# Kernel optimization log

Measured on AMD Instinct MI355X. Metric: run time of the kernel, lower is better.

The kernel has to match this reference:

```python
import jax, jax.numpy as jnp
import numpy as np

N_X, DIS, IN, OUT = 40000, 10000, 128, 64
N = N_X + DIS
E = 800000
BN_EPS = 1e-5


def setup_inputs() -> dict:
    key = jax.random.key(0)
    ks = jax.random.split(key, 20)

    def glorot(k, shape):
        fan_in, fan_out = shape[-2], shape[-1]
        a = np.sqrt(6.0 / (fan_in + fan_out)).astype(np.float32)
        return jax.random.uniform(k, shape, jnp.float32, -a, a)

    return {
        "x": jax.random.normal(ks[0], (N_X, IN), jnp.float32),
        "emb": jax.random.uniform(ks[1], (DIS, IN), jnp.float32),
        "conv1_w": glorot(ks[2], (3, IN, 2 * OUT)),
        "conv1_root": glorot(ks[3], (IN, 2 * OUT)),
        "conv1_bias": jnp.zeros((2 * OUT,), jnp.float32),
        "conv2_w": glorot(ks[4], (3, 2 * OUT, 4 * OUT)),
        "conv2_root": glorot(ks[5], (2 * OUT, 4 * OUT)),
        "conv2_bias": jnp.zeros((4 * OUT,), jnp.float32),
        "convinf_w": glorot(ks[6], (3, 4 * OUT, 4 * OUT)),
        "convinf_root": glorot(ks[7], (4 * OUT, 4 * OUT)),
        "convinf_bias": jnp.zeros((4 * OUT,), jnp.float32),
        "conv3_w": glorot(ks[8], (3, 4 * OUT, OUT)),
        "conv3_root": glorot(ks[9], (4 * OUT, OUT)),
        "conv3_bias": jnp.zeros((OUT,), jnp.float32),
        "norm1_g": jnp.ones((2 * OUT,), jnp.float32),
        "norm1_b": jnp.zeros((2 * OUT,), jnp.float32),
        "norm2_g": jnp.ones((4 * OUT,), jnp.float32),
        "norm2_b": jnp.zeros((4 * OUT,), jnp.float32),
        "edge_index": jax.random.randint(ks[10], (2, E), 0, N),
        "edge_types": jax.random.randint(ks[11], (E,), 0, 3),
    }


def reference(x, emb, conv1_w, conv1_root, conv1_bias, conv2_w, conv2_root,
              conv2_bias, convinf_w, convinf_root, convinf_bias, conv3_w,
              conv3_root, conv3_bias, norm1_g, norm1_b, norm2_g, norm2_b,
              edge_index, edge_types):
    dst, src = edge_index[0], edge_index[1]  # adj_t row = target, col = source
    n = x.shape[0] + emb.shape[0]

    # gcn_norm without self-loops: deg over rows, w_e = d^-1/2[dst] * d^-1/2[src]
    deg = jax.ops.segment_sum(jnp.ones(dst.shape[0], jnp.float32), dst, num_segments=n)
    dis = jnp.where(deg > 0, jax.lax.rsqrt(jnp.maximum(deg, 1.0)), 0.0)
    ew = dis[dst] * dis[src]  # [E]

    def wrgcn(h, W, root, bias):
        out = h @ root + bias
        h_src = h[src]  # [E, d] gather (dominant memory traffic)
        for r in range(3):
            w_r = jnp.where(edge_types == r, ew, 0.0)
            agg = jax.ops.segment_sum(w_r[:, None] * h_src, dst, num_segments=n)
            out = out + agg @ W[r]
        return out

    def bn(h, g, b):
        m = h.mean(axis=0)
        v = jnp.var(h, axis=0)  # biased, matches torch BN training normalization
        return (h - m) * jax.lax.rsqrt(v + BN_EPS) * g + b

    h0 = jnp.concatenate([x, emb], axis=0)  # [N, IN]
    x1 = bn(wrgcn(h0, conv1_w, conv1_root, conv1_bias), norm1_g, norm1_b)
    x2 = bn(wrgcn(jax.nn.relu(x1), conv2_w, conv2_root, conv2_bias), norm2_g, norm2_b)
    for _ in range(5):
        x2 = bn(wrgcn(jax.nn.relu(x2), convinf_w, convinf_root, convinf_bias), norm2_g, norm2_b)
    return wrgcn(jax.nn.relu(x2), conv3_w, conv3_root, conv3_bias)
```

## Files before the change

### kernel.cpp

```cpp
#include <hip/hip_runtime.h>

#define N_X  40000
#define NN   50000
#define NE   800000
#define MPAD 50048

using short8  = __attribute__((ext_vector_type(8))) short;
using floatx4 = __attribute__((ext_vector_type(4))) float;
using uintx2  = __attribute__((ext_vector_type(2))) unsigned int;
using uintx4  = __attribute__((ext_vector_type(4))) unsigned int;

typedef const __attribute__((address_space(1))) void gv_t;
typedef __attribute__((address_space(3))) void lv_t;

__device__ __forceinline__ unsigned short f2bf(float f) {
  unsigned u = __float_as_uint(f);
  u += 0x7FFF + ((u >> 16) & 1);
  return (unsigned short)(u >> 16);
}
__device__ __forceinline__ float bf2f(unsigned v) {
  return __uint_as_float(v << 16);
}
__device__ __forceinline__ float h2f(unsigned v) {
  unsigned short s = (unsigned short)v;
  _Float16 f;
  __builtin_memcpy(&f, &s, 2);
  return (float)f;
}
__device__ __forceinline__ unsigned short f2h(float f) {
  _Float16 h = (_Float16)f;
  unsigned short s;
  __builtin_memcpy(&s, &h, 2);
  return s;
}

__global__ void k_deg(const int* __restrict__ dst, int* __restrict__ deg) {
  int e = blockIdx.x * blockDim.x + threadIdx.x;
  if (e < NE) atomicAdd(&deg[dst[e]], 1);
}

__global__ void k_dis(const int* __restrict__ deg, float* __restrict__ dis) {
  int i = blockIdx.x * blockDim.x + threadIdx.x;
  if (i < NN) dis[i] = deg[i] > 0 ? rsqrtf((float)deg[i]) : 0.f;
}

#define SCAN_B 1024
#define SCAN_NB 49
__global__ void k_scan1(const int* __restrict__ deg, int* __restrict__ rowp,
                        int* __restrict__ bsum) {
  __shared__ int buf[SCAN_B];
  int b = blockIdx.x;
  int i = b * SCAN_B + threadIdx.x;
  int v = (i < NN) ? deg[i] : 0;
  buf[threadIdx.x] = v;
  __syncthreads();
  for (int off = 1; off < SCAN_B; off <<= 1) {
    int t = (threadIdx.x >= off) ? buf[threadIdx.x - off] : 0;
    __syncthreads();
    buf[threadIdx.x] += t;
    __syncthreads();
  }
  if (i < NN) rowp[i] = buf[threadIdx.x] - v;
  if (threadIdx.x == SCAN_B - 1) bsum[b] = buf[SCAN_B - 1];
}

__global__ void k_scan2(int* __restrict__ bsum) {
  if (threadIdx.x == 0) {
    int acc = 0;
    for (int i = 0; i < SCAN_NB; ++i) { int t = bsum[i]; bsum[i] = acc; acc += t; }
  }
}

__global__ void k_scan3(int* __restrict__ rowp, const int* __restrict__ bsum) {
  int i = blockIdx.x * blockDim.x + threadIdx.x;
  if (i < NN) rowp[i] += bsum[i >> 10];
  if (i == 0) rowp[NN] = NE;
}

__global__ void k_build(const int* __restrict__ dst, const int* __restrict__ src,
                        const int* __restrict__ typ, const float* __restrict__ dis,
                        const int* __restrict__ rowp, int* __restrict__ cur,
                        uintx2* __restrict__ ed) {
  int e = blockIdx.x * blockDim.x + threadIdx.x;
  if (e >= NE) return;
  int d = dst[e], s = src[e];
  int p = rowp[d] + atomicAdd(&cur[d], 1);
  uintx2 v;
  v.x = (unsigned)s | ((unsigned)typ[e] << 28);
  v.y = __float_as_uint(dis[d] * dis[s]);
  ed[p] = v;
}

__global__ void k_prep0(const float* __restrict__ x, const float* __restrict__ emb,
                        unsigned short* __restrict__ Gh, unsigned short* __restrict__ Gl) {
  int idx = blockIdx.x * blockDim.x + threadIdx.x;
  if (idx >= NN * 32) return;
  int r = idx >> 5;
  const float* srcp = (r < N_X) ? (x + (size_t)idx * 4)
                                : (emb + ((size_t)idx - (size_t)N_X * 32) * 4);
  float4 hv = *(const float4*)srcp;
  float vv[4] = {hv.x, hv.y, hv.z, hv.w};
  unsigned hw[2], lw[2];
#pragma unroll
  for (int q = 0; q < 2; ++q) {
    unsigned short h0 = f2bf(vv[2 * q]), h1 = f2bf(vv[2 * q + 1]);
    unsigned short l0 = f2bf(vv[2 * q] - bf2f(h0)), l1 = f2bf(vv[2 * q + 1] - bf2f(h1));
    hw[q] = (unsigned)h0 | ((unsigned)h1 << 16);
    lw[q] = (unsigned)l0 | ((unsigned)l1 << 16);
  }
  size_t o = (size_t)idx * 4;
  *(uintx2*)(Gh + o) = uintx2{hw[0], hw[1]};
  *(uintx2*)(Gl + o) = uintx2{lw[0], lw[1]};
}

__global__ void k_prep(const unsigned short* __restrict__ Hb,
                       const float* __restrict__ bns, const float* __restrict__ g,
                       const float* __restrict__ b, unsigned short* __restrict__ Gh,
                       unsigned short* __restrict__ Gl, int din) {
  int idx = blockIdx.x * blockDim.x + threadIdx.x;
  if (idx >= NN * (din >> 3)) return;
  int c8 = (idx & ((din >> 3) - 1)) * 8;
  uintx4 hv = *(const uintx4*)(Hb + (size_t)idx * 8);
  unsigned hwv[4] = {hv.x, hv.y, hv.z, hv.w};
  unsigned hw[4], lw[4];
#pragma unroll
  for (int q = 0; q < 4; ++q) {
    unsigned short oo[2];
#pragma unroll
    for (int p = 0; p < 2; ++p) {
      int c = c8 + 2 * q + p;
      float mean = bns[c] * (1.f / NN);
      float var = bns[din + c] * (1.f / NN) - mean * mean;
      float rs = rsqrtf(var + 1e-5f);
      float sc = rs * g[c];
      float sh = b[c] - mean * sc;
      float v = bf2f((hwv[q] >> (16 * p)) & 0xFFFFu);
      v = fmaxf(v * sc + sh, 0.f);
      oo[p] = f2bf(v);
      float lo = v - bf2f(oo[p]);
      if (p == 0) lw[q] = (unsigned)f2bf(lo);
      else        lw[q] |= ((unsigned)f2bf(lo) << 16);
    }
    hw[q] = (unsigned)oo[0] | ((unsigned)oo[1] << 16);
  }
  size_t o = (size_t)idx * 8;
  *(uintx4*)(Gh + o) = uintx4{hw[0], hw[1], hw[2], hw[3]};
  *(uintx4*)(Gl + o) = uintx4{lw[0], lw[1], lw[2], lw[3]};
}

__global__ void k_wcat2(const float* __restrict__ root, const float* __restrict__ W,
                        unsigned short* __restrict__ BhT, unsigned short* __restrict__ BlT,
                        int din, int dout) {
  int idx = blockIdx.x * blockDim.x + threadIdx.x;
  if (idx >= 4 * dout * din) return;
  int n = idx / din, k = idx % din;
  float v;
  if (n < dout) v = root[(size_t)k * dout + n];
  else {
    int r = n / dout - 1, c = n % dout;
    v = W[((size_t)r * din + k) * dout + c];
  }
  unsigned short h = f2bf(v);
  BhT[idx] = h;
  BlT[idx] = f2bf(v - bf2f(h));
}

__global__ __launch_bounds__(256, 2) void k_gemm2(
    const unsigned short* __restrict__ Ah, const unsigned short* __restrict__ Al,
    const unsigned short* __restrict__ Bh, const unsigned short* __restrict__ Bl,
    float* __restrict__ Rroot, unsigned short* __restrict__ P,
    int M, int K, int dout, int ny) {
  constexpr int TC = 40;
  constexpr int CPW = 10;
  constexpr int NT = 2;
  __shared__ __align__(16) char lds[2][TC * 1024];

  const int tid = threadIdx.x;
  const int lane = tid & 63;
  const int w = tid >> 6;
  const int wm = w >> 1, wn = w & 1;
  const int r16 = lane & 15, kg = lane >> 4;

  const int nwg = gridDim.x;
  const int q = nwg >> 3, r = nwg & 7;
  const int xcd = blockIdx.x & 7, pos = blockIdx.x >> 3;
  const int t = (xcd < r ? xcd * (q + 1) : r * (q + 1) + (xcd - r) * q) + pos;
  const int bm = (t / ny) * 256;
  const int bn = (t % ny) * 64;

  const int rowseg = lane >> 2;
  const int seg = (lane & 3) ^ ((lane >> 3) & 3);
  const unsigned short* gb[CPW];
#pragma unroll
  for (int i = 0; i < CPW; ++i) {
    int c = w * CPW + i;
    const unsigned short* base;
    int row0;
    if (c < 16)      { base = Ah; row0 = bm + c * 16; }
    else if (c < 32) { base = Al; row0 = bm + (c - 16) * 16; }
    else if (c < 36) { base = Bh; row0 = bn + (c - 32) * 16; }
    else             { base = Bl; row0 = bn + (c - 36) * 16; }
    gb[i] = base + (size_t)(row0 + rowseg) * K + seg * 8;
  }

  floatx4 acc[8][NT];
#pragma unroll
  for (int i = 0; i < 8; ++i)
#pragma unroll
    for (int jj = 0; jj < NT; ++jj) acc[i][jj] = (floatx4)0.f;

  const int nk = K >> 5;

  auto stage = [&](int b, int tk) {
#pragma unroll
    for (int i = 0; i < CPW; ++i)
      __builtin_amdgcn_global_load_lds((gv_t*)(gb[i] + tk * 32),
                                       (lv_t*)&lds[b][(w * CPW + i) * 1024],
                                       16, 0, 0);
  };

  stage(0, 0);
  stage(1, 1);

  const int fo = r16 * 64 + ((kg ^ ((r16 >> 1) & 3)) * 16);

  int buf = 0;
  for (int tk = 0; tk < nk; ++tk) {
    if (tk < nk - 1) asm volatile("s_waitcnt vmcnt(10)" ::: "memory");
    else             asm volatile("s_waitcnt vmcnt(0)" ::: "memory");
    __builtin_amdgcn_s_barrier();

    const char* Lb = lds[buf];
    short8 bh[NT], bl[NT];
#pragma unroll
    for (int nt = 0; nt < NT; ++nt) {
      bh[nt] = *(const short8*)(Lb + (32 + wn * NT + nt) * 1024 + fo);
      bl[nt] = *(const short8*)(Lb + (36 + wn * NT + nt) * 1024 + fo);
    }

    __builtin_amdgcn_s_setprio(1);
#pragma unroll
    for (int mt = 0; mt < 8; ++mt) {
      short8 ah = *(const short8*)(Lb + (wm * 8 + mt) * 1024 + fo);
      short8 al = *(const short8*)(Lb + (16 + wm * 8 + mt) * 1024 + fo);
#pragma unroll
      for (int nt = 0; nt < NT; ++nt) {
        acc[mt][nt] = __builtin_amdgcn_mfma_f32_16x16x32_bf16(ah, bh[nt], acc[mt][nt], 0, 0, 0);
        acc[mt][nt] = __builtin_amdgcn_mfma_f32_16x16x32_bf16(ah, bl[nt], acc[mt][nt], 0, 0, 0);
        acc[mt][nt] = __builtin_amdgcn_mfma_f32_16x16x32_bf16(al, bh[nt], acc[mt][nt], 0, 0, 0);
      }
    }
    __builtin_amdgcn_s_setprio(0);

    __builtin_amdgcn_s_barrier();
    if (tk + 2 < nk) stage(buf, tk + 2);
    buf ^= 1;
  }

  const int sec = bn / dout;
  const int cb = bn - sec * dout;
#pragma unroll
  for (int mt = 0; mt < 8; ++mt) {
    const int gr0 = bm + wm * 128 + mt * 16 + kg * 4;
#pragma unroll
    for (int nt = 0; nt < NT; ++nt) {
      const int colL = cb + wn * 32 + nt * 16 + r16;
#pragma unroll
      for (int rr = 0; rr < 4; ++rr) {
        const int gr = gr0 + rr;
        if (gr >= M) continue;
        const float o = acc[mt][nt][rr];
        if (sec == 0) Rroot[(size_t)gr * dout + colL] = o;
        else          P[((size_t)gr * 3 + (sec - 1)) * dout + colL] = f2h(o);
      }
    }
  }
}

template <int L, bool F32OUT>
__global__ void k_agg2(const unsigned short* __restrict__ P,
                       const float* __restrict__ Rroot,
                       const float* __restrict__ bias,
                       const int* __restrict__ rowp, const uintx2* __restrict__ ed,
                       void* __restrict__ OutV) {
  constexpr int G = 64 / L;
  constexpr int dout = L * 8;
  const int wid = (blockIdx.x * 256 + threadIdx.x) >> 6;
  if (wid >= NN) return;
  const int lane = threadIdx.x & 63;
  const int grp = lane / L;
  const int c0 = (lane & (L - 1)) * 8;
  const int beg = rowp[wid], end = rowp[wid + 1];
  float a[8] = {};
  for (int i = beg + grp; i < end; i += G) {
    const uintx2 e = ed[i];
    const float wv = __uint_as_float(e.y);
    const unsigned tt = e.x >> 28;
    const size_t off = ((size_t)(e.x & 0x0FFFFFFFu) * 3 + tt) * dout + c0;
    const uintx4 g = *(const uintx4*)(P + off);
    a[0] += wv * h2f(g.x & 0xFFFFu);
    a[1] += wv * h2f(g.x >> 16);
    a[2] += wv * h2f(g.y & 0xFFFFu);
    a[3] += wv * h2f(g.y >> 16);
    a[4] += wv * h2f(g.z & 0xFFFFu);
    a[5] += wv * h2f(g.z >> 16);
    a[6] += wv * h2f(g.w & 0xFFFFu);
    a[7] += wv * h2f(g.w >> 16);
  }
#pragma unroll
  for (int off = L; off < 64; off <<= 1) {
#pragma unroll
    for (int qq = 0; qq < 8; ++qq) a[qq] += __shfl_xor(a[qq], off);
  }
  if (grp == 0) {
    const size_t ob = (size_t)wid * dout + c0;
    const float4 bv0 = *(const float4*)(bias + c0);
    const float4 bv1 = *(const float4*)(bias + c0 + 4);
    const float4 rv0 = *(const float4*)(Rroot + ob);
    const float4 rv1 = *(const float4*)(Rroot + ob + 4);
    float o[8];
    o[0] = rv0.x + bv0.x + a[0];
    o[1] = rv0.y + bv0.y + a[1];
    o[2] = rv0.z + bv0.z + a[2];
    o[3] = rv0.w + bv0.w + a[3];
    o[4] = rv1.x + bv1.x + a[4];
    o[5] = rv1.y + bv1.y + a[5];
    o[6] = rv1.z + bv1.z + a[6];
    o[7] = rv1.w + bv1.w + a[7];
    if constexpr (F32OUT) {
      float* Out = (float*)OutV;
      *(float4*)(Out + ob) = make_float4(o[0], o[1], o[2], o[3]);
      *(float4*)(Out + ob + 4) = make_float4(o[4], o[5], o[6], o[7]);
    } else {
      unsigned short* Out = (unsigned short*)OutV;
      uintx4 pk;
      pk.x = (unsigned)f2bf(o[0]) | ((unsigned)f2bf(o[1]) << 16);
      pk.y = (unsigned)f2bf(o[2]) | ((unsigned)f2bf(o[3]) << 16);
      pk.z = (unsigned)f2bf(o[4]) | ((unsigned)f2bf(o[5]) << 16);
      pk.w = (unsigned)f2bf(o[6]) | ((unsigned)f2bf(o[7]) << 16);
      *(uintx4*)(Out + ob) = pk;
    }
  }
}

__global__ void k_bnstats(const unsigned short* __restrict__ Hb,
                          float* __restrict__ sums, int d) {
  int c = threadIdx.x;
  float s = 0.f, s2 = 0.f;
  for (int r = blockIdx.x; r < NN; r += gridDim.x) {
    float v = bf2f(Hb[(size_t)r * d + c]);
    s += v;
    s2 += v * v;
  }
  atomicAdd(&sums[c], s);
  atomicAdd(&sums[d + c], s2);
}

extern "C" void kernel_launch(void* const* d_in, const int* in_sizes, int n_in,
                              void* d_out, int out_size, void* d_ws, size_t ws_size,
                              hipStream_t stream) {
  const float* x   = (const float*)d_in[0];
  const float* emb = (const float*)d_in[1];
  const float* conv_w[4] = {(const float*)d_in[2], (const float*)d_in[5],
                            (const float*)d_in[8], (const float*)d_in[11]};
  const float* conv_r[4] = {(const float*)d_in[3], (const float*)d_in[6],
                            (const float*)d_in[9], (const float*)d_in[12]};
  const float* conv_b[4] = {(const float*)d_in[4], (const float*)d_in[7],
                            (const float*)d_in[10], (const float*)d_in[13]};
  const float* n1g = (const float*)d_in[14];
  const float* n1b = (const float*)d_in[15];
  const float* n2g = (const float*)d_in[16];
  const float* n2b = (const float*)d_in[17];
  const int* eidx = (const int*)d_in[18];
  const int* etyp = (const int*)d_in[19];
  const int* dst  = eidx;
  const int* srcp = eidx + NE;
  float* out = (float*)d_out;

  char* w = (char*)d_ws;
  auto alloc = [&](size_t bytes) {
    char* p = w;
    w += (bytes + 255) & ~(size_t)255;
    return p;
  };
  unsigned short* Gh   = (unsigned short*)alloc((size_t)MPAD * 256 * 2);
  unsigned short* Gl   = (unsigned short*)alloc((size_t)MPAD * 256 * 2);
  unsigned short* P    = (unsigned short*)alloc((size_t)MPAD * 768 * 2);
  float*    Rroot = (float*)alloc((size_t)MPAD * 256 * 4);
  unsigned short* Hb = (unsigned short*)alloc((size_t)NN * 256 * 2);
  unsigned short* WTh[4];
  unsigned short* WTl[4];
  for (int i = 0; i < 4; ++i) {
    WTh[i] = (unsigned short*)alloc((size_t)1024 * 256 * 2);
    WTl[i] = (unsigned short*)alloc((size_t)1024 * 256 * 2);
  }
  float*    bns  = (float*)alloc(512 * 4);
  float*    dis  = (float*)alloc((size_t)NN * 4);
  int*      deg  = (int*)alloc((size_t)NN * 4);
  int*      rowp = (int*)alloc((size_t)(NN + 1) * 4);
  int*      cur  = (int*)alloc((size_t)NN * 4);
  int*      bsum = (int*)alloc(64 * 4);
  uintx2*   ed   = (uintx2*)alloc((size_t)NE * 8);

  hipMemsetAsync(deg, 0, (size_t)NN * 4, stream);
  hipMemsetAsync(cur, 0, (size_t)NN * 4, stream);
  k_deg<<<(NE + 255) / 256, 256, 0, stream>>>(dst, deg);
  k_dis<<<(NN + 255) / 256, 256, 0, stream>>>(deg, dis);
  k_scan1<<<SCAN_NB, SCAN_B, 0, stream>>>(deg, rowp, bsum);
  k_scan2<<<1, 64, 0, stream>>>(bsum);
  k_scan3<<<(NN + 255) / 256, 256, 0, stream>>>(rowp, bsum);
  k_build<<<(NE + 255) / 256, 256, 0, stream>>>(dst, srcp, etyp, dis, rowp, cur, ed);

  const int din_a[8]  = {128, 128, 256, 256, 256, 256, 256, 256};
  const int dout_a[8] = {128, 256, 256, 256, 256, 256, 256, 64};
  const int wi_a[8]   = {0, 1, 2, 2, 2, 2, 2, 3};
  const int gm = (MPAD + 255) / 256;

  const int wdin[4]  = {128, 128, 256, 256};
  const int wdout[4] = {128, 256, 256, 64};
  for (int i = 0; i < 4; ++i)
    k_wcat2<<<(4 * wdout[i] * wdin[i] + 255) / 256, 256, 0, stream>>>(
        conv_r[i], conv_w[i], WTh[i], WTl[i], wdin[i], wdout[i]);

  for (int l = 0; l < 8; ++l) {
    const int din = din_a[l], dout = dout_a[l];
    const int wi = wi_a[l];

    if (l == 0)
      k_prep0<<<(NN * 32 + 255) / 256, 256, 0, stream>>>(x, emb, Gh, Gl);
    else
      k_prep<<<(NN * (din >> 3) + 255) / 256, 256, 0, stream>>>(
          Hb, bns, (l == 1) ? n1g : n2g, (l == 1) ? n1b : n2b, Gh, Gl, din);

    const int ny = 4 * dout / 64;
    k_gemm2<<<gm * ny, 256, 0, stream>>>(Gh, Gl, WTh[wi], WTl[wi], Rroot, P, NN, din, dout, ny);

    if (l == 7) {
      k_agg2<8, true><<<(NN + 3) / 4, 256, 0, stream>>>(P, Rroot, conv_b[wi], rowp, ed, out);
    } else {
      if (dout == 256)
        k_agg2<32, false><<<(NN + 3) / 4, 256, 0, stream>>>(P, Rroot, conv_b[wi], rowp, ed, Hb);
      else
        k_agg2<16, false><<<(NN + 3) / 4, 256, 0, stream>>>(P, Rroot, conv_b[wi], rowp, ed, Hb);
      hipMemsetAsync(bns, 0, (size_t)2 * dout * 4, stream);
      k_bnstats<<<256, dout, 0, stream>>>(Hb, bns, dout);
    }
  }
}
```

Measured before the change: 1.711 ms.

## Preload B weight fragments into registers and template GEMM on K

The GEMM kernel now loads the full K-extent of the B (weight) hi/lo fragments directly from global memory into registers at kernel start, instead of staging them through LDS each K-step. The A tiles are still staged through LDS with double buffering, so the LDS footprint shrinks from 40 to 32 chunks per buffer and the vmcnt wait count is adjusted to match. K is made a template parameter so the K-loop fully unrolls. This removes per-iteration B LDS traffic and barriers' share of it, but raises register pressure considerably (up to 8x2x2 short8 for K=256), which may spill or limit occupancy under launch_bounds(256,2).

```diff
diff --git a/kernel.cpp b/kernel.cpp
--- a/kernel.cpp
+++ b/kernel.cpp
@@ -165,13 +165,15 @@
   BlT[idx] = f2bf(v - bf2f(h));
 }
 
-__global__ __launch_bounds__(256, 2) void k_gemm2(
+template <int NK>
+__global__ __launch_bounds__(256, 2) void k_gemm3(
     const unsigned short* __restrict__ Ah, const unsigned short* __restrict__ Al,
     const unsigned short* __restrict__ Bh, const unsigned short* __restrict__ Bl,
     float* __restrict__ Rroot, unsigned short* __restrict__ P,
-    int M, int K, int dout, int ny) {
-  constexpr int TC = 40;
-  constexpr int CPW = 10;
+    int M, int dout, int ny) {
+  constexpr int K = NK * 32;
+  constexpr int TC = 32;
+  constexpr int CPW = 8;
   constexpr int NT = 2;
   __shared__ __align__(16) char lds[2][TC * 1024];
 
@@ -188,18 +190,25 @@
   const int bm = (t / ny) * 256;
   const int bn = (t % ny) * 64;
 
+  short8 bf[NK][NT][2];
+#pragma unroll
+  for (int tk = 0; tk < NK; ++tk)
+#pragma unroll
+    for (int nt = 0; nt < NT; ++nt) {
+      const int row = bn + wn * 32 + nt * 16 + r16;
+      const size_t bo = (size_t)row * K + tk * 32 + kg * 8;
+      bf[tk][nt][0] = *(const short8*)(Bh + bo);
+      bf[tk][nt][1] = *(const short8*)(Bl + bo);
+    }
+
   const int rowseg = lane >> 2;
   const int seg = (lane & 3) ^ ((lane >> 3) & 3);
   const unsigned short* gb[CPW];
 #pragma unroll
   for (int i = 0; i < CPW; ++i) {
     int c = w * CPW + i;
-    const unsigned short* base;
-    int row0;
-    if (c < 16)      { base = Ah; row0 = bm + c * 16; }
-    else if (c < 32) { base = Al; row0 = bm + (c - 16) * 16; }
-    else if (c < 36) { base = Bh; row0 = bn + (c - 32) * 16; }
-    else             { base = Bl; row0 = bn + (c - 36) * 16; }
+    const unsigned short* base = (c < 16) ? Ah : Al;
+    int row0 = bm + (c & 15) * 16;
     gb[i] = base + (size_t)(row0 + rowseg) * K + seg * 8;
   }
 
@@ -208,8 +217,6 @@
   for (int i = 0; i < 8; ++i)
 #pragma unroll
     for (int jj = 0; jj < NT; ++jj) acc[i][jj] = (floatx4)0.f;
-
-  const int nk = K >> 5;
 
   auto stage = [&](int b, int tk) {
 #pragma unroll
@@ -220,24 +227,18 @@
   };
 
   stage(0, 0);
-  stage(1, 1);
+  if (NK > 1) stage(1, 1);
 
   const int fo = r16 * 64 + ((kg ^ ((r16 >> 1) & 3)) * 16);
 
   int buf = 0;
-  for (int tk = 0; tk < nk; ++tk) {
-    if (tk < nk - 1) asm volatile("s_waitcnt vmcnt(10)" ::: "memory");
+#pragma unroll
+  for (int tk = 0; tk < NK; ++tk) {
+    if (tk < NK - 1) asm volatile("s_waitcnt vmcnt(8)" ::: "memory");
     else             asm volatile("s_waitcnt vmcnt(0)" ::: "memory");
     __builtin_amdgcn_s_barrier();
 
     const char* Lb = lds[buf];
-    short8 bh[NT], bl[NT];
-#pragma unroll
-    for (int nt = 0; nt < NT; ++nt) {
-      bh[nt] = *(const short8*)(Lb + (32 + wn * NT + nt) * 1024 + fo);
-      bl[nt] = *(const short8*)(Lb + (36 + wn * NT + nt) * 1024 + fo);
-    }
-
     __builtin_amdgcn_s_setprio(1);
 #pragma unroll
     for (int mt = 0; mt < 8; ++mt) {
@@ -245,15 +246,15 @@
       short8 al = *(const short8*)(Lb + (16 + wm * 8 + mt) * 1024 + fo);
 #pragma unroll
       for (int nt = 0; nt < NT; ++nt) {
-        acc[mt][nt] = __builtin_amdgcn_mfma_f32_16x16x32_bf16(ah, bh[nt], acc[mt][nt], 0, 0, 0);
-        acc[mt][nt] = __builtin_amdgcn_mfma_f32_16x16x32_bf16(ah, bl[nt], acc[mt][nt], 0, 0, 0);
-        acc[mt][nt] = __builtin_amdgcn_mfma_f32_16x16x32_bf16(al, bh[nt], acc[mt][nt], 0, 0, 0);
+        acc[mt][nt] = __builtin_amdgcn_mfma_f32_16x16x32_bf16(ah, bf[tk][nt][0], acc[mt][nt], 0, 0, 0);
+        acc[mt][nt] = __builtin_amdgcn_mfma_f32_16x16x32_bf16(ah, bf[tk][nt][1], acc[mt][nt], 0, 0, 0);
+        acc[mt][nt] = __builtin_amdgcn_mfma_f32_16x16x32_bf16(al, bf[tk][nt][0], acc[mt][nt], 0, 0, 0);
       }
     }
     __builtin_amdgcn_s_setprio(0);
 
     __builtin_amdgcn_s_barrier();
-    if (tk + 2 < nk) stage(buf, tk + 2);
+    if (tk + 2 < NK) stage(buf, tk + 2);
     buf ^= 1;
   }
 
@@ -433,7 +434,10 @@
           Hb, bns, (l == 1) ? n1g : n2g, (l == 1) ? n1b : n2b, Gh, Gl, din);
 
     const int ny = 4 * dout / 64;
-    k_gemm2<<<gm * ny, 256, 0, stream>>>(Gh, Gl, WTh[wi], WTl[wi], Rroot, P, NN, din, dout, ny);
+    if (din == 128)
+      k_gemm3<4><<<gm * ny, 256, 0, stream>>>(Gh, Gl, WTh[wi], WTl[wi], Rroot, P, NN, dout, ny);
+    else
+      k_gemm3<8><<<gm * ny, 256, 0, stream>>>(Gh, Gl, WTh[wi], WTl[wi], Rroot, P, NN, dout, ny);
 
     if (l == 7) {
       k_agg2<8, true><<<(NN + 3) / 4, 256, 0, stream>>>(P, Rroot, conv_b[wi], rowp, ed, out);
```

Measured after the change: 1.815 ms. 6.1% more time.
